# Optimization experiments

Measured on AMD Instinct MI355X. Metric: run time of the kernel, lower is better.

The kernel has to match this reference:

```python
import jax, jax.numpy as jnp
import numpy as np

# Longformer-base-like config, 4 layers, seq 2048, one-sided window 256 (attention_window=512)
B, S, DM, H, L, FF, V, WIN = 1, 2048, 768, 12, 4, 3072, 50265, 256


def _ln(x, s, b):
    m = x.mean(-1, keepdims=True)
    v = ((x - m) ** 2).mean(-1, keepdims=True)
    return (x - m) * jax.lax.rsqrt(v + 1e-5) * s + b


def setup_inputs() -> dict:
    key = jax.random.key(0)
    ks = iter(jax.random.split(key, 48))
    nrm = lambda shape: jax.random.normal(next(ks), shape, jnp.float32) * 0.02
    z = lambda shape: jnp.zeros(shape, jnp.float32)
    o = lambda shape: jnp.ones(shape, jnp.float32)
    return {
        'src': jax.random.randint(next(ks), (B, S), 0, V),
        'mask_src': jnp.ones((B, S), jnp.int32),
        'cluster_sizes': jax.random.randint(next(ks), (B,), 1, 10),
        'emb_word': nrm((V, DM)), 'emb_pos': nrm((S + 2, DM)),
        'ln_emb_s': o((DM,)), 'ln_emb_b': z((DM,)),
        'Wq': nrm((L, DM, DM)), 'bq': z((L, DM)),
        'Wk': nrm((L, DM, DM)), 'bk': z((L, DM)),
        'Wv': nrm((L, DM, DM)), 'bv': z((L, DM)),
        'Wo': nrm((L, DM, DM)), 'bo': z((L, DM)),
        'Wqg': nrm((L, DM, DM)), 'bqg': z((L, DM)),
        'Wkg': nrm((L, DM, DM)), 'bkg': z((L, DM)),
        'Wvg': nrm((L, DM, DM)), 'bvg': z((L, DM)),
        'ln1_s': o((L, DM)), 'ln1_b': z((L, DM)),
        'Wff1': nrm((L, DM, FF)), 'bff1': z((L, FF)),
        'Wff2': nrm((L, FF, DM)), 'bff2': z((L, DM)),
        'ln2_s': o((L, DM)), 'ln2_b': z((L, DM)),
        'Wcls': nrm((DM,)), 'bcls': z(()),
    }


def _encode(src, mask_src, emb_word, emb_pos, ln_emb_s, ln_emb_b,
            Wq, bq, Wk, bk, Wv, bv, Wo, bo, Wqg, bqg, Wkg, bkg, Wvg, bvg,
            ln1_s, ln1_b, Wff1, bff1, Wff2, bff2, ln2_s, ln2_b):
    Dh = DM // H
    NC = S // WIN  # number of query chunks
    NEG = jnp.float32(-1e9)
    scale = jnp.float32(1.0 / np.sqrt(Dh))
    mask_f = mask_src.astype(jnp.float32)

    # RoBERTa-style embeddings (positions offset by padding_idx+1 = 2)
    x = _ln(emb_word[src] + emb_pos[jnp.arange(S) + 2][None], ln_emb_s, ln_emb_b)

    # Banded gather indices: chunk c of W queries sees 3W keys [c*W - W, c*W + 2W)
    idx = jnp.arange(NC)[:, None] * WIN + jnp.arange(3 * WIN)[None, :]  # [NC,3W] into padded seq
    j_abs = idx - WIN                                                   # absolute key positions
    qi = jnp.arange(NC)[:, None] * WIN + jnp.arange(WIN)[None, :]       # [NC,W] absolute query pos
    rel = j_abs[:, None, :] - qi[:, :, None]                            # [NC,W,3W]
    in_band = (jnp.abs(rel) <= WIN) & (j_abs[:, None, :] >= 0) & (j_abs[:, None, :] < S)
    # keys removed from windowed attention: padding tokens and global tokens (position 0)
    key_ok = mask_f * (jnp.arange(S)[None, :] != 0)                     # [B,S]
    kmb = jnp.pad(key_ok, ((0, 0), (WIN, WIN)))[:, idx]                 # [B,NC,3W]
    band_ok = in_band[None, None] & (kmb[:, None, :, None, :] > 0)      # [B,1,NC,W,3W]

    for l in range(L):
        heads = lambda Wm, bm: (x @ Wm[l] + bm[l]).reshape(B, S, H, Dh).transpose(0, 2, 1, 3)
        q = heads(Wq, bq) * scale                                       # [B,H,S,Dh]
        k = heads(Wk, bk)
        v = heads(Wv, bv)
        kb = jnp.pad(k, ((0, 0), (0, 0), (WIN, WIN), (0, 0)))[:, :, idx]  # [B,H,NC,3W,Dh]
        vb = jnp.pad(v, ((0, 0), (0, 0), (WIN, WIN), (0, 0)))[:, :, idx]
        band = jnp.einsum('bhcqd,bhckd->bhcqk', q.reshape(B, H, NC, WIN, Dh), kb)
        band = jnp.where(band_ok, band, NEG)
        # every query also attends the global key (position 0) via the regular k/v
        sg = jnp.einsum('bhsd,bhd->bhs', q, k[:, :, 0])
        sg = jnp.where((mask_f[:, 0] > 0)[:, None, None], sg, NEG).reshape(B, H, NC, WIN, 1)
        probs = jax.nn.softmax(jnp.concatenate([sg, band], axis=-1), axis=-1)
        pg = probs[..., 0].reshape(B, H, S)
        out = jnp.einsum('bhcqk,bhckd->bhcqd', probs[..., 1:], vb).reshape(B, H, S, Dh)
        out = out + pg[..., None] * v[:, :, 0][:, :, None, :]
        # global query token (position 0): full attention using the *_global projections
        qg = ((x[:, 0] @ Wqg[l] + bqg[l]).reshape(B, H, Dh)) * scale
        kg = heads(Wkg, bkg)
        vg = heads(Wvg, bvg)
        sgl = jnp.where(mask_f[:, None, :] > 0, jnp.einsum('bhd,bhsd->bhs', qg, kg), NEG)
        og = jnp.einsum('bhs,bhsd->bhd', jax.nn.softmax(sgl, axis=-1), vg)
        out = out.at[:, :, 0].set(og)
        ctx = out.transpose(0, 2, 1, 3).reshape(B, S, DM)
        x = _ln(x + ctx @ Wo[l] + bo[l], ln1_s[l], ln1_b[l])
        ff = jax.nn.gelu(x @ Wff1[l] + bff1[l], approximate=False) @ Wff2[l] + bff2[l]
        x = _ln(x + ff, ln2_s[l], ln2_b[l])
    return x


def reference(src, mask_src, cluster_sizes, emb_word, emb_pos, ln_emb_s, ln_emb_b,
              Wq, bq, Wk, bk, Wv, bv, Wo, bo, Wqg, bqg, Wkg, bkg, Wvg, bvg,
              ln1_s, ln1_b, Wff1, bff1, Wff2, bff2, ln2_s, ln2_b, Wcls, bcls):
    x = _encode(src, mask_src, emb_word, emb_pos, ln_emb_s, ln_emb_b,
                Wq, bq, Wk, bk, Wv, bv, Wo, bo, Wqg, bqg, Wkg, bkg, Wvg, bvg,
                ln1_s, ln1_b, Wff1, bff1, Wff2, bff2, ln2_s, ln2_b)
    mask0 = mask_src[:, 0].astype(jnp.float32)
    scores = jax.nn.sigmoid(x[:, 0] @ Wcls + bcls) * mask0  # Classifier on CLS embedding
    return scores[:, None], mask_src[:, 0][:, None]
```

## Files before the change

### kernel.cpp

```cpp
#include <hip/hip_runtime.h>
#include <hip/hip_bf16.h>
#include <math.h>

#define S_LEN 2048
#define DMODEL 768
#define NHEAD 12
#define DHEAD 64
#define NLAYER 4
#define FFDIM 3072
#define WINSZ 256

typedef unsigned short u16;
typedef __attribute__((ext_vector_type(8))) short bfrag;
typedef __attribute__((ext_vector_type(4))) float ffrag;

static __device__ __forceinline__ int detect_bf16(const unsigned* flagp) {
    return flagp[0] != 0x3F800000u;
}

static __device__ __forceinline__ float ldin(const void* p, long i, int bf) {
    return bf ? __bfloat162float(((const __hip_bfloat16*)p)[i])
              : ((const float*)p)[i];
}

static __device__ __forceinline__ u16 f2bf(float v) {
    unsigned u = __float_as_uint(v);
    unsigned r = (u + 0x7FFFu + ((u >> 16) & 1u)) >> 16;
    return (u16)r;
}

static __device__ __forceinline__ float bf2f(u16 v) {
    return __uint_as_float((unsigned)v << 16);
}

static __device__ __forceinline__ void async16(const u16* g, u16* l) {
#if __has_builtin(__builtin_amdgcn_global_load_lds)
    __builtin_amdgcn_global_load_lds(
        (const __attribute__((address_space(1))) void*)g,
        (__attribute__((address_space(3))) void*)l, 16, 0, 0);
#else
    *(int4*)l = *(const int4*)g;
#endif
}

static __device__ __forceinline__ void blk_reduce_sum2(float& a, float& b) {
    __shared__ float sred[8];
    #pragma unroll
    for (int off = 32; off; off >>= 1) {
        a += __shfl_down(a, off);
        b += __shfl_down(b, off);
    }
    int lane = threadIdx.x & 63, w = threadIdx.x >> 6;
    if (lane == 0) { sred[w] = a; sred[w + 4] = b; }
    __syncthreads();
    a = sred[0] + sred[1] + sred[2] + sred[3];
    b = sred[4] + sred[5] + sred[6] + sred[7];
    __syncthreads();
}

struct T6Args { const void* w[6]; };

__global__ __launch_bounds__(256)
void transpose_w6_kernel(T6Args args, u16* __restrict__ Wt,
                         const unsigned* __restrict__ flagp) {
    int bf = detect_bf16(flagp);
    int z = blockIdx.z;
    const void* W = args.w[z >> 2];
    long so = (long)(z & 3) * DMODEL * DMODEL;
    long dofs = (long)z * DMODEL * DMODEL;
    int n0 = blockIdx.x * 64, k0 = blockIdx.y * 64;
    __shared__ float t[64][65];
    int tid = threadIdx.x;
    #pragma unroll
    for (int r = 0; r < 16; ++r) {
        int idx = r * 256 + tid;
        int k = idx >> 6, n = idx & 63;
        t[k][n] = ldin(W, so + (long)(k0 + k) * DMODEL + n0 + n, bf);
    }
    __syncthreads();
    #pragma unroll
    for (int r = 0; r < 16; ++r) {
        int idx = r * 256 + tid;
        int n = idx >> 6, k = idx & 63;
        Wt[dofs + (long)(n0 + n) * DMODEL + k0 + k] = f2bf(t[k][n]);
    }
}

__global__ __launch_bounds__(256)
void transpose_w_kernel(const void* __restrict__ W, u16* __restrict__ Wt,
                        int K, int N, const unsigned* __restrict__ flagp) {
    int bf = detect_bf16(flagp);
    long zo = (long)blockIdx.z * K * N;
    int n0 = blockIdx.x * 64, k0 = blockIdx.y * 64;
    __shared__ float t[64][65];
    int tid = threadIdx.x;
    #pragma unroll
    for (int r = 0; r < 16; ++r) {
        int idx = r * 256 + tid;
        int k = idx >> 6, n = idx & 63;
        t[k][n] = ldin(W, zo + (long)(k0 + k) * N + n0 + n, bf);
    }
    __syncthreads();
    #pragma unroll
    for (int r = 0; r < 16; ++r) {
        int idx = r * 256 + tid;
        int n = idx >> 6, k = idx & 63;
        Wt[zo + (long)(n0 + n) * K + k0 + k] = f2bf(t[k][n]);
    }
}

__global__ __launch_bounds__(256)
void embed_kernel(const int* __restrict__ src, const void* __restrict__ emb_word,
                  const void* __restrict__ emb_pos, const void* __restrict__ ln_s,
                  const void* __restrict__ ln_b, float* __restrict__ X,
                  u16* __restrict__ Xb, const unsigned* __restrict__ flagp) {
    int bf = detect_bf16(flagp);
    int s = blockIdx.x;
    int tid = threadIdx.x;
    int tok = src[s];
    float e[3];
    #pragma unroll
    for (int i = 0; i < 3; ++i) {
        int d = tid + i * 256;
        e[i] = ldin(emb_word, (long)tok * DMODEL + d, bf)
             + ldin(emb_pos, (long)(s + 2) * DMODEL + d, bf);
    }
    float sum = e[0] + e[1] + e[2];
    float sq  = e[0]*e[0] + e[1]*e[1] + e[2]*e[2];
    blk_reduce_sum2(sum, sq);
    float mean = sum * (1.0f / DMODEL);
    float var  = sq * (1.0f / DMODEL) - mean * mean;
    float inv  = rsqrtf(var + 1e-5f);
    #pragma unroll
    for (int i = 0; i < 3; ++i) {
        int d = tid + i * 256;
        float v = (e[i] - mean) * inv * ldin(ln_s, d, bf) + ldin(ln_b, d, bf);
        X[(long)s * DMODEL + d] = v;
        Xb[(long)s * DMODEL + d] = f2bf(v);
    }
}

__global__ __launch_bounds__(256)
void ln_res2_kernel(float* __restrict__ X, const float* __restrict__ T0,
                    const float* __restrict__ T1,
                    const void* __restrict__ ln_s, long soff,
                    const void* __restrict__ ln_b, long boff,
                    u16* __restrict__ Xb, const unsigned* __restrict__ flagp) {
    int bf = detect_bf16(flagp);
    int s = blockIdx.x;
    int tid = threadIdx.x;
    float e[3];
    #pragma unroll
    for (int i = 0; i < 3; ++i) {
        long d = (long)s * DMODEL + tid + i * 256;
        e[i] = X[d] + T0[d] + T1[d];
    }
    float sum = e[0] + e[1] + e[2];
    float sq  = e[0]*e[0] + e[1]*e[1] + e[2]*e[2];
    blk_reduce_sum2(sum, sq);
    float mean = sum * (1.0f / DMODEL);
    float var  = sq * (1.0f / DMODEL) - mean * mean;
    float inv  = rsqrtf(var + 1e-5f);
    #pragma unroll
    for (int i = 0; i < 3; ++i) {
        int d = tid + i * 256;
        float v = (e[i] - mean) * inv * ldin(ln_s, soff + d, bf) + ldin(ln_b, boff + d, bf);
        X[(long)s * DMODEL + d] = v;
        Xb[(long)s * DMODEL + d] = f2bf(v);
    }
}

static __device__ __forceinline__ void gemm_body(
    const u16* __restrict__ A, int lda, const u16* __restrict__ Wt, int ldb,
    const void* __restrict__ bias, long boff, int bf,
    float* __restrict__ outF, u16* __restrict__ outB, u16* __restrict__ outBT, int ldt,
    int N, int klen, float alpha, int gelu,
    u16 (*As)[32], u16 (*Bs)[32], int bm, int bn)
{
    int tid = threadIdx.x;
    int wave = tid >> 6, lane = tid & 63;
    int quad = lane >> 4, l15 = lane & 15;
    int wm = (wave >> 1) * 64, wn = (wave & 1) * 64;

    int srow = wave * 16 + (lane >> 2);
    int scol = (lane & 3) * 8;
    const u16* Ag0 = A  + (long)(bm + srow) * lda + scol;
    const u16* Ag1 = A  + (long)(bm + 64 + srow) * lda + scol;
    const u16* Bg0 = Wt + (long)(bn + srow) * ldb + scol;
    const u16* Bg1 = Wt + (long)(bn + 64 + srow) * ldb + scol;
    u16* Al0 = &As[srow][scol];
    u16* Al1 = &As[64 + srow][scol];
    u16* Bl0 = &Bs[srow][scol];
    u16* Bl1 = &Bs[64 + srow][scol];

    ffrag zero = {0.f, 0.f, 0.f, 0.f};
    ffrag acc[4][4];
    #pragma unroll
    for (int mi = 0; mi < 4; ++mi)
        #pragma unroll
        for (int ni = 0; ni < 4; ++ni) acc[mi][ni] = zero;

    for (int k0 = 0; k0 < klen; k0 += 32) {
        __syncthreads();
        async16(Ag0 + k0, Al0);
        async16(Ag1 + k0, Al1);
        async16(Bg0 + k0, Bl0);
        async16(Bg1 + k0, Bl1);
        __syncthreads();
        bfrag af[4], bfr[4];
        #pragma unroll
        for (int mi = 0; mi < 4; ++mi)
            af[mi] = *(const bfrag*)&As[wm + mi * 16 + l15][quad * 8];
        #pragma unroll
        for (int ni = 0; ni < 4; ++ni)
            bfr[ni] = *(const bfrag*)&Bs[wn + ni * 16 + l15][quad * 8];
        #pragma unroll
        for (int mi = 0; mi < 4; ++mi)
            #pragma unroll
            for (int ni = 0; ni < 4; ++ni)
                acc[mi][ni] = __builtin_amdgcn_mfma_f32_16x16x32_bf16(
                    af[mi], bfr[ni], acc[mi][ni], 0, 0, 0);
    }

    #pragma unroll
    for (int mi = 0; mi < 4; ++mi) {
        #pragma unroll
        for (int ni = 0; ni < 4; ++ni) {
            int row0 = bm + wm + mi * 16 + quad * 4;
            int col  = bn + wn + ni * 16 + l15;
            float bb = bias ? ldin(bias, boff + col, bf) : 0.0f;
            float v[4];
            #pragma unroll
            for (int i = 0; i < 4; ++i) {
                float x = (acc[mi][ni][i] + bb) * alpha;
                if (gelu) x = 0.5f * x * (1.0f + erff(x * 0.70710678118f));
                v[i] = x;
            }
            if (outF) {
                #pragma unroll
                for (int i = 0; i < 4; ++i) outF[(long)(row0 + i) * N + col] = v[i];
            }
            if (outB) {
                #pragma unroll
                for (int i = 0; i < 4; ++i) outB[(long)(row0 + i) * N + col] = f2bf(v[i]);
            }
            if (outBT) {
                ushort4 pk;
                pk.x = f2bf(v[0]); pk.y = f2bf(v[1]); pk.z = f2bf(v[2]); pk.w = f2bf(v[3]);
                *(ushort4*)&outBT[(long)col * ldt + row0] = pk;
            }
        }
    }
}

__global__ __launch_bounds__(256)
void gemm_one_kernel(const u16* __restrict__ A, int lda, const u16* __restrict__ Wt, int ldb,
                     const void* __restrict__ bias, long boff,
                     float* __restrict__ outF, long ofstride, u16* __restrict__ outB,
                     int N, int klen, float alpha, int gelu,
                     const unsigned* __restrict__ flagp) {
    __shared__ __align__(16) u16 As[128][32];
    __shared__ __align__(16) u16 Bs[128][32];
    long kbeg = (long)blockIdx.z * klen;
    gemm_body(A + kbeg, lda, Wt + kbeg, ldb,
              blockIdx.z == 0 ? bias : nullptr, boff, detect_bf16(flagp),
              outF ? outF + blockIdx.z * ofstride : nullptr, outB, nullptr, 0,
              N, klen, alpha, gelu, As, Bs, blockIdx.x * 128, blockIdx.y * 128);
}

struct Qkv5Args {
    const u16* wt[5];
    const void* bias[5];
    u16* outB[5];
    u16* outBT[5];
};

__global__ __launch_bounds__(256)
void gemm_qkv5_kernel(const u16* __restrict__ A, Qkv5Args args, long boff,
                      const unsigned* __restrict__ flagp) {
    __shared__ __align__(16) u16 As[128][32];
    __shared__ __align__(16) u16 Bs[128][32];
    int z = blockIdx.z;
    float alpha = (z == 0) ? 0.125f : 1.0f;
    gemm_body(A, DMODEL, args.wt[z], DMODEL, args.bias[z], boff, detect_bf16(flagp),
              nullptr, args.outB[z], args.outBT[z], S_LEN,
              DMODEL, DMODEL, alpha, 0,
              As, Bs, blockIdx.x * 128, blockIdx.y * 128);
}

__global__ __launch_bounds__(256)
void qg_kernel(const float* __restrict__ X, const void* __restrict__ W, long woff,
               float* __restrict__ QGp, const unsigned* __restrict__ flagp) {
    int bf = detect_bf16(flagp);
    int colb = blockIdx.x * 128, kb = blockIdx.y * 96;
    int cl = threadIdx.x & 127, kh = threadIdx.x >> 7;
    int col = colb + cl;
    __shared__ float xs[96];
    __shared__ float acc2[128];
    if (threadIdx.x < 96) xs[threadIdx.x] = X[kb + threadIdx.x];
    __syncthreads();
    float a = 0.0f;
    #pragma unroll 4
    for (int k = kh * 48; k < kh * 48 + 48; ++k)
        a = fmaf(xs[k], ldin(W, woff + (long)(kb + k) * DMODEL + col, bf), a);
    if (kh) acc2[cl] = a;
    __syncthreads();
    if (!kh) QGp[(long)blockIdx.y * DMODEL + col] = a + acc2[cl];
}

__global__ __launch_bounds__(256)
void band_mfma_kernel(const u16* __restrict__ Qb, const u16* __restrict__ Kb,
                      const u16* __restrict__ Vtg, u16* __restrict__ CTXb) {
    int qt = blockIdx.x, h = blockIdx.y;
    int q0 = qt * 64;
    int tid = threadIdx.x;
    int wave = tid >> 6, lane = tid & 63;
    int quad = lane >> 4, l15 = lane & 15;

    __shared__ __align__(16) u16 Qs[64][72];
    __shared__ __align__(16) u16 Ks[64][72];
    __shared__ __align__(16) u16 Vs[64][72];
    __shared__ __align__(16) float Pb[4][16][68];
    __shared__ __align__(16) u16 k0s[64];
    __shared__ __align__(16) u16 v0s[64];

    {
        int r = tid >> 2, seg = tid & 3;
        const u16* gq = Qb + (long)(q0 + r) * DMODEL + h * DHEAD + seg * 16;
        *(int4*)&Qs[r][seg * 16]     = *(const int4*)gq;
        *(int4*)&Qs[r][seg * 16 + 8] = *(const int4*)(gq + 8);
        if (tid < 8) *(int4*)&k0s[tid * 8] = *(const int4*)(Kb + h * DHEAD + tid * 8);
        if (tid >= 64 && tid < 128) {
            int d = tid - 64;
            v0s[d] = Vtg[(long)(h * DHEAD + d) * S_LEN];
        }
    }
    __syncthreads();

    float part = 0.0f;
    #pragma unroll
    for (int j = 0; j < 16; ++j)
        part = fmaf(bf2f(Qs[wave * 16 + l15][quad * 16 + j]), bf2f(k0s[quad * 16 + j]), part);
    part += __shfl_xor(part, 16);
    part += __shfl_xor(part, 32);
    float m = part, l = 1.0f;

    ffrag O4[4];
    #pragma unroll
    for (int dt = 0; dt < 4; ++dt) {
        float vv = bf2f(v0s[dt * 16 + l15]);
        ffrag t = {vv, vv, vv, vv};
        O4[dt] = t;
    }

    bfrag bq[2];
    bq[0] = *(const bfrag*)&Qs[wave * 16 + l15][quad * 8];
    bq[1] = *(const bfrag*)&Qs[wave * 16 + l15][32 + quad * 8];

    int q_abs = q0 + wave * 16 + l15;
    float (*Pw)[68] = Pb[wave];

    for (int t = 0; t < 9; ++t) {
        int jb = q0 - 256 + t * 64;
        if (jb < 0 || jb >= S_LEN) continue;

        __syncthreads();
        {
            int r = tid >> 2, seg = tid & 3;
            const u16* gk = Kb + (long)(jb + r) * DMODEL + h * DHEAD + seg * 16;
            *(int4*)&Ks[r][seg * 16]     = *(const int4*)gk;
            *(int4*)&Ks[r][seg * 16 + 8] = *(const int4*)(gk + 8);
            const u16* gv = Vtg + (long)(h * DHEAD + r) * S_LEN + jb + seg * 16;
            *(int4*)&Vs[r][seg * 16]     = *(const int4*)gv;
            *(int4*)&Vs[r][seg * 16 + 8] = *(const int4*)(gv + 8);
        }
        __syncthreads();

        ffrag sa[4];
        #pragma unroll
        for (int mt = 0; mt < 4; ++mt) {
            bfrag a0 = *(const bfrag*)&Ks[mt * 16 + l15][quad * 8];
            bfrag a1 = *(const bfrag*)&Ks[mt * 16 + l15][32 + quad * 8];
            ffrag z = {0.f, 0.f, 0.f, 0.f};
            z = __builtin_amdgcn_mfma_f32_16x16x32_bf16(a0, bq[0], z, 0, 0, 0);
            z = __builtin_amdgcn_mfma_f32_16x16x32_bf16(a1, bq[1], z, 0, 0, 0);
            sa[mt] = z;
        }

        float mx = -3e38f;
        #pragma unroll
        for (int mt = 0; mt < 4; ++mt) {
            #pragma unroll
            for (int reg = 0; reg < 4; ++reg) {
                int key = jb + mt * 16 + quad * 4 + reg;
                int rel = key - q_abs;
                bool ok = (key >= 1) && (rel >= -WINSZ) && (rel <= WINSZ);
                float s = ok ? sa[mt][reg] : -1e30f;
                sa[mt][reg] = s;
                mx = fmaxf(mx, s);
            }
        }
        mx = fmaxf(mx, __shfl_xor(mx, 16));
        mx = fmaxf(mx, __shfl_xor(mx, 32));
        float m_new = fmaxf(m, mx);
        float alpha = __expf(m - m_new);

        float rs = 0.0f;
        #pragma unroll
        for (int mt = 0; mt < 4; ++mt) {
            #pragma unroll
            for (int reg = 0; reg < 4; ++reg) {
                float p = __expf(sa[mt][reg] - m_new);
                sa[mt][reg] = p;
                rs += p;
            }
        }
        rs += __shfl_xor(rs, 16);
        rs += __shfl_xor(rs, 32);
        l = l * alpha + rs;
        m = m_new;

        #pragma unroll
        for (int mt = 0; mt < 4; ++mt)
            #pragma unroll
            for (int reg = 0; reg < 4; ++reg)
                Pw[l15][mt * 16 + quad * 4 + reg] = sa[mt][reg];

        float a4[4];
        #pragma unroll
        for (int reg = 0; reg < 4; ++reg)
            a4[reg] = __shfl(alpha, (lane & 48) + quad * 4 + reg);

        bfrag pa[2];
        #pragma unroll
        for (int ks = 0; ks < 2; ++ks) {
            float4 f0 = *(const float4*)&Pw[l15][ks * 32 + quad * 8];
            float4 f1 = *(const float4*)&Pw[l15][ks * 32 + quad * 8 + 4];
            union { bfrag v; short s[8]; } pu;
            pu.s[0] = (short)f2bf(f0.x); pu.s[1] = (short)f2bf(f0.y);
            pu.s[2] = (short)f2bf(f0.z); pu.s[3] = (short)f2bf(f0.w);
            pu.s[4] = (short)f2bf(f1.x); pu.s[5] = (short)f2bf(f1.y);
            pu.s[6] = (short)f2bf(f1.z); pu.s[7] = (short)f2bf(f1.w);
            pa[ks] = pu.v;
        }

        #pragma unroll
        for (int dt = 0; dt < 4; ++dt) {
            bfrag v0f = *(const bfrag*)&Vs[dt * 16 + l15][quad * 8];
            bfrag v1f = *(const bfrag*)&Vs[dt * 16 + l15][32 + quad * 8];
            ffrag o = O4[dt];
            #pragma unroll
            for (int reg = 0; reg < 4; ++reg) o[reg] *= a4[reg];
            o = __builtin_amdgcn_mfma_f32_16x16x32_bf16(pa[0], v0f, o, 0, 0, 0);
            o = __builtin_amdgcn_mfma_f32_16x16x32_bf16(pa[1], v1f, o, 0, 0, 0);
            O4[dt] = o;
        }
    }

    float l4[4];
    #pragma unroll
    for (int reg = 0; reg < 4; ++reg)
        l4[reg] = __shfl(l, (lane & 48) + quad * 4 + reg);

    #pragma unroll
    for (int dt = 0; dt < 4; ++dt) {
        #pragma unroll
        for (int reg = 0; reg < 4; ++reg) {
            int row = q0 + wave * 16 + quad * 4 + reg;
            CTXb[(long)row * DMODEL + h * DHEAD + dt * 16 + l15] = f2bf(O4[dt][reg] / l4[reg]);
        }
    }
}

__global__ __launch_bounds__(256)
void gattn_part_kernel(const float* __restrict__ QGp, const void* __restrict__ bqg, long boff,
                       const u16* __restrict__ KG, const u16* __restrict__ VG,
                       float* __restrict__ Gml, float* __restrict__ GO,
                       const unsigned* __restrict__ flagp) {
    int h = blockIdx.x, ck = blockIdx.y;
    int tid = threadIdx.x;
    int bf = detect_bf16(flagp);
    __shared__ float qs[DHEAD];
    __shared__ float sc[256];
    __shared__ float red[4];
    __shared__ float pt[4][DHEAD];

    if (tid < DHEAD) {
        float a = 0.0f;
        #pragma unroll
        for (int z = 0; z < 8; ++z) a += QGp[(long)z * DMODEL + h * DHEAD + tid];
        qs[tid] = (a + ldin(bqg, boff + h * DHEAD + tid, bf)) * 0.125f;
    }
    __syncthreads();

    int s = ck * 256 + tid;
    const int4* kp = (const int4*)(KG + (long)s * DMODEL + h * DHEAD);
    float dsum = 0.0f;
    #pragma unroll
    for (int i = 0; i < 8; ++i) {
        int4 raw = kp[i];
        const u16* pr = (const u16*)&raw;
        #pragma unroll
        for (int j = 0; j < 8; ++j) dsum = fmaf(qs[i * 8 + j], bf2f(pr[j]), dsum);
    }
    sc[tid] = dsum;
    float v = dsum;
    #pragma unroll
    for (int off = 32; off; off >>= 1) v = fmaxf(v, __shfl_down(v, off));
    if ((tid & 63) == 0) red[tid >> 6] = v;
    __syncthreads();
    float M = fmaxf(fmaxf(red[0], red[1]), fmaxf(red[2], red[3]));
    __syncthreads();
    float e = __expf(dsum - M);
    sc[tid] = e;
    float sum = e;
    #pragma unroll
    for (int off = 32; off; off >>= 1) sum += __shfl_down(sum, off);
    if ((tid & 63) == 0) red[tid >> 6] = sum;
    __syncthreads();
    float L = red[0] + red[1] + red[2] + red[3];

    int g = tid >> 6, dd = tid & 63;
    float acc = 0.0f;
    for (int j = g * 64; j < g * 64 + 64; ++j)
        acc = fmaf(sc[j], bf2f(VG[(long)(ck * 256 + j) * DMODEL + h * DHEAD + dd]), acc);
    pt[g][dd] = acc;
    __syncthreads();
    if (tid < DHEAD)
        GO[((long)h * 8 + ck) * DHEAD + tid] = pt[0][tid] + pt[1][tid] + pt[2][tid] + pt[3][tid];
    if (tid == 0) {
        Gml[((long)h * 8 + ck) * 2]     = M;
        Gml[((long)h * 8 + ck) * 2 + 1] = L;
    }
}

__global__ __launch_bounds__(64)
void gattn_combine_kernel(const float* __restrict__ Gml, const float* __restrict__ GO,
                          u16* __restrict__ CTXb) {
    int h = blockIdx.x, d = threadIdx.x;
    float M = -3e38f;
    #pragma unroll
    for (int z = 0; z < 8; ++z) M = fmaxf(M, Gml[((long)h * 8 + z) * 2]);
    float L = 0.0f, O = 0.0f;
    #pragma unroll
    for (int z = 0; z < 8; ++z) {
        float w = __expf(Gml[((long)h * 8 + z) * 2] - M);
        L += Gml[((long)h * 8 + z) * 2 + 1] * w;
        O = fmaf(GO[((long)h * 8 + z) * DHEAD + d], w, O);
    }
    CTXb[h * DHEAD + d] = f2bf(O / L);
}

__global__ __launch_bounds__(256)
void cls_kernel(const float* __restrict__ X, const void* __restrict__ Wcls,
                const void* __restrict__ bcls, const int* __restrict__ mask_src,
                void* __restrict__ out, const unsigned* __restrict__ flagp) {
    int bf = detect_bf16(flagp);
    int tid = threadIdx.x;
    float a = 0.0f, dummy = 0.0f;
    #pragma unroll
    for (int i = 0; i < 3; ++i) {
        int d = tid + i * 256;
        a = fmaf(X[d], ldin(Wcls, d, bf), a);
    }
    blk_reduce_sum2(a, dummy);
    if (tid == 0) {
        float z = a + ldin(bcls, 0, bf);
        float scr = 1.0f / (1.0f + __expf(-z));
        float mk = (float)mask_src[0];
        scr *= mk;
        if (bf) {
            __hip_bfloat16* o = (__hip_bfloat16*)out;
            o[0] = __float2bfloat16(scr);
            o[1] = __float2bfloat16(mk);
        } else {
            float* o = (float*)out;
            o[0] = scr;
            o[1] = mk;
        }
    }
}

extern "C" void kernel_launch(void* const* d_in, const int* in_sizes, int n_in,
                              void* d_out, int out_size, void* d_ws, size_t ws_size,
                              hipStream_t stream) {
    (void)in_sizes; (void)n_in; (void)out_size; (void)ws_size;
    const int* src       = (const int*)d_in[0];
    const int* mask_src  = (const int*)d_in[1];
    const void* emb_word = d_in[3];
    const void* emb_pos  = d_in[4];
    const unsigned* flagp = (const unsigned*)d_in[5];
    const void* ln_emb_s = d_in[5];
    const void* ln_emb_b = d_in[6];

    char* base = (char*)d_ws;
    size_t off = 0;
    auto carve = [&](size_t bytes) {
        void* p = base + off;
        off = (off + bytes + 255) & ~(size_t)255;
        return p;
    };
    const long DD = (long)DMODEL * DMODEL;
    const long DF = (long)DMODEL * FFDIM;
    const long SD = (long)S_LEN * DMODEL;
    const long SF = (long)S_LEN * FFDIM;

    u16* W6    = (u16*)carve(6 * NLAYER * DD * 2);
    u16* FF1T  = (u16*)carve(NLAYER * DF * 2);
    u16* FF2T  = (u16*)carve(NLAYER * DF * 2);
    float* X   = (float*)carve(SD * 4);
    float* TMP0 = (float*)carve(SD * 4);
    float* TMP1 = (float*)carve(SD * 4);
    u16* Xb    = (u16*)carve(SD * 2);
    u16* Qb16  = (u16*)carve(SD * 2);
    u16* Kb16  = (u16*)carve(SD * 2);
    u16* Vtg   = (u16*)carve(SD * 2);
    u16* KGb16 = (u16*)carve(SD * 2);
    u16* VGb16 = (u16*)carve(SD * 2);
    u16* CTXb  = (u16*)carve(SD * 2);
    u16* FF1b  = (u16*)carve(SF * 2);
    float* QGp = (float*)carve(8 * DMODEL * 4);
    float* Gml = (float*)carve(NHEAD * 8 * 2 * 4);
    float* GO  = (float*)carve(NHEAD * 8 * DHEAD * 4);

    T6Args t6;
    t6.w[0] = d_in[7];  t6.w[1] = d_in[9];  t6.w[2] = d_in[11];
    t6.w[3] = d_in[17]; t6.w[4] = d_in[19]; t6.w[5] = d_in[13];
    transpose_w6_kernel<<<dim3(12, 12, 24), 256, 0, stream>>>(t6, W6, flagp);
    transpose_w_kernel<<<dim3(48, 12, NLAYER), 256, 0, stream>>>(d_in[23], FF1T, DMODEL, FFDIM, flagp);
    transpose_w_kernel<<<dim3(12, 48, NLAYER), 256, 0, stream>>>(d_in[25], FF2T, FFDIM, DMODEL, flagp);

    embed_kernel<<<S_LEN, 256, 0, stream>>>(src, emb_word, emb_pos, ln_emb_s, ln_emb_b,
                                            X, Xb, flagp);

    for (int l = 0; l < NLAYER; ++l) {
        long wo  = (long)l * DD;
        long bo  = (long)l * DMODEL;
        long b1o = (long)l * FFDIM;

        Qkv5Args qa;
        qa.wt[0] = W6 + (0L * NLAYER + l) * DD; qa.bias[0] = d_in[8];  qa.outB[0] = Qb16;  qa.outBT[0] = nullptr;
        qa.wt[1] = W6 + (1L * NLAYER + l) * DD; qa.bias[1] = d_in[10]; qa.outB[1] = Kb16;  qa.outBT[1] = nullptr;
        qa.wt[2] = W6 + (2L * NLAYER + l) * DD; qa.bias[2] = d_in[12]; qa.outB[2] = nullptr; qa.outBT[2] = Vtg;
        qa.wt[3] = W6 + (3L * NLAYER + l) * DD; qa.bias[3] = d_in[18]; qa.outB[3] = KGb16; qa.outBT[3] = nullptr;
        qa.wt[4] = W6 + (4L * NLAYER + l) * DD; qa.bias[4] = d_in[20]; qa.outB[4] = VGb16; qa.outBT[4] = nullptr;
        gemm_qkv5_kernel<<<dim3(16, 6, 5), 256, 0, stream>>>(Xb, qa, bo, flagp);

        qg_kernel<<<dim3(6, 8), 256, 0, stream>>>(X, d_in[15], wo, QGp, flagp);

        band_mfma_kernel<<<dim3(32, NHEAD), 256, 0, stream>>>(Qb16, Kb16, Vtg, CTXb);
        gattn_part_kernel<<<dim3(NHEAD, 8), 256, 0, stream>>>(QGp, d_in[16], bo, KGb16, VGb16,
                                                              Gml, GO, flagp);
        gattn_combine_kernel<<<NHEAD, 64, 0, stream>>>(Gml, GO, CTXb);

        gemm_one_kernel<<<dim3(16, 6, 2), 256, 0, stream>>>(
            CTXb, DMODEL, W6 + (5L * NLAYER + l) * DD, DMODEL, d_in[14], bo,
            TMP0, SD, nullptr, DMODEL, 384, 1.0f, 0, flagp);
        ln_res2_kernel<<<S_LEN, 256, 0, stream>>>(X, TMP0, TMP1, d_in[21], bo, d_in[22], bo, Xb, flagp);

        gemm_one_kernel<<<dim3(16, 24, 1), 256, 0, stream>>>(
            Xb, DMODEL, FF1T + (long)l * DF, DMODEL, d_in[24], b1o,
            nullptr, 0, FF1b, FFDIM, DMODEL, 1.0f, 1, flagp);
        gemm_one_kernel<<<dim3(16, 6, 2), 256, 0, stream>>>(
            FF1b, FFDIM, FF2T + (long)l * DF, FFDIM, d_in[26], bo,
            TMP0, SD, nullptr, DMODEL, 1536, 1.0f, 0, flagp);
        ln_res2_kernel<<<S_LEN, 256, 0, stream>>>(X, TMP0, TMP1, d_in[27], bo, d_in[28], bo, Xb, flagp);
    }

    cls_kernel<<<1, 256, 0, stream>>>(X, d_in[29], d_in[30], mask_src, d_out, flagp);
}
```

Baseline: 1.087 ms.

## Fuse attention kernels, transposes, global-combine and classifier to cut launches

Merges the three weight-transpose launches into one flat-grid kernel. Merges the query-global projection, banded attention and global partial attention into a single kernel that uses a shared-memory union. The global-attention combine is folded into the Wo GEMM as a patch of row 0 of the A tile, and the classifier is folded into the final layernorm. This removes several small kernel launches and serial dependencies per layer, at the cost of extra branches and syncthreads inside the GEMM loop and a serial global-q projection inside each global block.

```diff
diff --git a/kernel.cpp b/kernel.cpp
--- a/kernel.cpp
+++ b/kernel.cpp
@@ -58,54 +58,45 @@
     __syncthreads();
 }
 
-struct T6Args { const void* w[6]; };
+struct TAllArgs { const void* w[8]; u16* d6; u16* d1; u16* d2; };
 
 __global__ __launch_bounds__(256)
-void transpose_w6_kernel(T6Args args, u16* __restrict__ Wt,
-                         const unsigned* __restrict__ flagp) {
+void transpose_all_kernel(TAllArgs args, const unsigned* __restrict__ flagp) {
     int bf = detect_bf16(flagp);
-    int z = blockIdx.z;
-    const void* W = args.w[z >> 2];
-    long so = (long)(z & 3) * DMODEL * DMODEL;
-    long dofs = (long)z * DMODEL * DMODEL;
-    int n0 = blockIdx.x * 64, k0 = blockIdx.y * 64;
+    const long DD = (long)DMODEL * DMODEL;
+    const long DF = (long)DMODEL * FFDIM;
+    int bid = blockIdx.x;
+    const void* srcp; u16* dst; int K, N, n0, k0; long so, dofs;
+    if (bid < 3456) {
+        int z = bid / 144, t = bid % 144;
+        srcp = args.w[z >> 2]; so = (long)(z & 3) * DD;
+        dst = args.d6; dofs = (long)z * DD;
+        K = DMODEL; N = DMODEL; n0 = (t % 12) * 64; k0 = (t / 12) * 64;
+    } else if (bid < 5760) {
+        int i = bid - 3456, layer = i / 576, t = i % 576;
+        srcp = args.w[6]; so = (long)layer * DF;
+        dst = args.d1; dofs = (long)layer * DF;
+        K = DMODEL; N = FFDIM; n0 = (t % 48) * 64; k0 = (t / 48) * 64;
+    } else {
+        int i = bid - 5760, layer = i / 576, t = i % 576;
+        srcp = args.w[7]; so = (long)layer * DF;
+        dst = args.d2; dofs = (long)layer * DF;
+        K = FFDIM; N = DMODEL; n0 = (t % 12) * 64; k0 = (t / 12) * 64;
+    }
     __shared__ float t[64][65];
     int tid = threadIdx.x;
     #pragma unroll
     for (int r = 0; r < 16; ++r) {
         int idx = r * 256 + tid;
         int k = idx >> 6, n = idx & 63;
-        t[k][n] = ldin(W, so + (long)(k0 + k) * DMODEL + n0 + n, bf);
+        t[k][n] = ldin(srcp, so + (long)(k0 + k) * N + n0 + n, bf);
     }
     __syncthreads();
     #pragma unroll
     for (int r = 0; r < 16; ++r) {
         int idx = r * 256 + tid;
         int n = idx >> 6, k = idx & 63;
-        Wt[dofs + (long)(n0 + n) * DMODEL + k0 + k] = f2bf(t[k][n]);
-    }
-}
-
-__global__ __launch_bounds__(256)
-void transpose_w_kernel(const void* __restrict__ W, u16* __restrict__ Wt,
-                        int K, int N, const unsigned* __restrict__ flagp) {
-    int bf = detect_bf16(flagp);
-    long zo = (long)blockIdx.z * K * N;
-    int n0 = blockIdx.x * 64, k0 = blockIdx.y * 64;
-    __shared__ float t[64][65];
-    int tid = threadIdx.x;
-    #pragma unroll
-    for (int r = 0; r < 16; ++r) {
-        int idx = r * 256 + tid;
-        int k = idx >> 6, n = idx & 63;
-        t[k][n] = ldin(W, zo + (long)(k0 + k) * N + n0 + n, bf);
-    }
-    __syncthreads();
-    #pragma unroll
-    for (int r = 0; r < 16; ++r) {
-        int idx = r * 256 + tid;
-        int n = idx >> 6, k = idx & 63;
-        Wt[zo + (long)(n0 + n) * K + k0 + k] = f2bf(t[k][n]);
+        dst[dofs + (long)(n0 + n) * K + k0 + k] = f2bf(t[k][n]);
     }
 }
 
@@ -145,7 +136,10 @@
                     const float* __restrict__ T1,
                     const void* __restrict__ ln_s, long soff,
                     const void* __restrict__ ln_b, long boff,
-                    u16* __restrict__ Xb, const unsigned* __restrict__ flagp) {
+                    u16* __restrict__ Xb, const unsigned* __restrict__ flagp,
+                    int do_cls, const void* __restrict__ Wcls,
+                    const void* __restrict__ bcls, const int* __restrict__ mask_src,
+                    void* __restrict__ out) {
     int bf = detect_bf16(flagp);
     int s = blockIdx.x;
     int tid = threadIdx.x;
@@ -161,12 +155,36 @@
     float mean = sum * (1.0f / DMODEL);
     float var  = sq * (1.0f / DMODEL) - mean * mean;
     float inv  = rsqrtf(var + 1e-5f);
+    float v3[3];
     #pragma unroll
     for (int i = 0; i < 3; ++i) {
         int d = tid + i * 256;
         float v = (e[i] - mean) * inv * ldin(ln_s, soff + d, bf) + ldin(ln_b, boff + d, bf);
+        v3[i] = v;
         X[(long)s * DMODEL + d] = v;
         Xb[(long)s * DMODEL + d] = f2bf(v);
+    }
+    if (do_cls && s == 0) {
+        float a = 0.0f, dummy = 0.0f;
+        #pragma unroll
+        for (int i = 0; i < 3; ++i)
+            a = fmaf(v3[i], ldin(Wcls, tid + i * 256, bf), a);
+        blk_reduce_sum2(a, dummy);
+        if (tid == 0) {
+            float z = a + ldin(bcls, 0, bf);
+            float scr = 1.0f / (1.0f + __expf(-z));
+            float mk = (float)mask_src[0];
+            scr *= mk;
+            if (bf) {
+                __hip_bfloat16* o = (__hip_bfloat16*)out;
+                o[0] = __float2bfloat16(scr);
+                o[1] = __float2bfloat16(mk);
+            } else {
+                float* o = (float*)out;
+                o[0] = scr;
+                o[1] = mk;
+            }
+        }
     }
 }
 
@@ -175,7 +193,8 @@
     const void* __restrict__ bias, long boff, int bf,
     float* __restrict__ outF, u16* __restrict__ outB, u16* __restrict__ outBT, int ldt,
     int N, int klen, float alpha, int gelu,
-    u16 (*As)[32], u16 (*Bs)[32], int bm, int bn)
+    u16 (*As)[32], u16 (*Bs)[32], int bm, int bn,
+    int patch_mode, const u16* __restrict__ ctx0s, long kbeg)
 {
     int tid = threadIdx.x;
     int wave = tid >> 6, lane = tid & 63;
@@ -207,6 +226,14 @@
         async16(Bg0 + k0, Bl0);
         async16(Bg1 + k0, Bl1);
         __syncthreads();
+        if (patch_mode) {
+            if (bm == 0 && tid < 4) {
+                #pragma unroll
+                for (int j = 0; j < 8; ++j)
+                    As[0][tid * 8 + j] = ctx0s[kbeg + k0 + tid * 8 + j];
+            }
+            __syncthreads();
+        }
         bfrag af[4], bfr[4];
         #pragma unroll
         for (int mi = 0; mi < 4; ++mi)
@@ -258,14 +285,35 @@
                      const void* __restrict__ bias, long boff,
                      float* __restrict__ outF, long ofstride, u16* __restrict__ outB,
                      int N, int klen, float alpha, int gelu,
+                     const float* __restrict__ Gml, const float* __restrict__ GO,
                      const unsigned* __restrict__ flagp) {
     __shared__ __align__(16) u16 As[128][32];
     __shared__ __align__(16) u16 Bs[128][32];
+    __shared__ __align__(16) u16 ctx0s[DMODEL];
+    int patch = (Gml != nullptr);
+    int bm = blockIdx.x * 128;
+    if (patch && bm == 0) {
+        for (int i = threadIdx.x; i < DMODEL; i += 256) {
+            int h = i >> 6, d = i & 63;
+            float M = -3e38f;
+            #pragma unroll
+            for (int z = 0; z < 8; ++z) M = fmaxf(M, Gml[((long)h * 8 + z) * 2]);
+            float L = 0.f, O = 0.f;
+            #pragma unroll
+            for (int z = 0; z < 8; ++z) {
+                float w = __expf(Gml[((long)h * 8 + z) * 2] - M);
+                L += Gml[((long)h * 8 + z) * 2 + 1] * w;
+                O = fmaf(GO[((long)h * 8 + z) * DHEAD + d], w, O);
+            }
+            ctx0s[i] = f2bf(O / L);
+        }
+    }
     long kbeg = (long)blockIdx.z * klen;
     gemm_body(A + kbeg, lda, Wt + kbeg, ldb,
               blockIdx.z == 0 ? bias : nullptr, boff, detect_bf16(flagp),
               outF ? outF + blockIdx.z * ofstride : nullptr, outB, nullptr, 0,
-              N, klen, alpha, gelu, As, Bs, blockIdx.x * 128, blockIdx.y * 128);
+              N, klen, alpha, gelu, As, Bs, bm, blockIdx.y * 128,
+              patch, ctx0s, kbeg);
 }
 
 struct Qkv5Args {
@@ -285,298 +333,250 @@
     gemm_body(A, DMODEL, args.wt[z], DMODEL, args.bias[z], boff, detect_bf16(flagp),
               nullptr, args.outB[z], args.outBT[z], S_LEN,
               DMODEL, DMODEL, alpha, 0,
-              As, Bs, blockIdx.x * 128, blockIdx.y * 128);
-}
+              As, Bs, blockIdx.x * 128, blockIdx.y * 128, 0, nullptr, 0);
+}
+
+struct BandShared {
+    u16 Qs[64][72];
+    u16 Ks[64][72];
+    u16 Vs[64][72];
+    float Pb[4][16][68];
+    u16 k0s[64];
+    u16 v0s[64];
+};
+struct GattnShared {
+    float xs[DMODEL];
+    float qs[DHEAD];
+    float sc[256];
+    float red[4];
+    float pt[4][DHEAD];
+};
+union AttnShared { BandShared b; GattnShared g; };
 
 __global__ __launch_bounds__(256)
-void qg_kernel(const float* __restrict__ X, const void* __restrict__ W, long woff,
-               float* __restrict__ QGp, const unsigned* __restrict__ flagp) {
-    int bf = detect_bf16(flagp);
-    int colb = blockIdx.x * 128, kb = blockIdx.y * 96;
-    int cl = threadIdx.x & 127, kh = threadIdx.x >> 7;
-    int col = colb + cl;
-    __shared__ float xs[96];
-    __shared__ float acc2[128];
-    if (threadIdx.x < 96) xs[threadIdx.x] = X[kb + threadIdx.x];
-    __syncthreads();
-    float a = 0.0f;
-    #pragma unroll 4
-    for (int k = kh * 48; k < kh * 48 + 48; ++k)
-        a = fmaf(xs[k], ldin(W, woff + (long)(kb + k) * DMODEL + col, bf), a);
-    if (kh) acc2[cl] = a;
-    __syncthreads();
-    if (!kh) QGp[(long)blockIdx.y * DMODEL + col] = a + acc2[cl];
-}
-
-__global__ __launch_bounds__(256)
-void band_mfma_kernel(const u16* __restrict__ Qb, const u16* __restrict__ Kb,
-                      const u16* __restrict__ Vtg, u16* __restrict__ CTXb) {
-    int qt = blockIdx.x, h = blockIdx.y;
-    int q0 = qt * 64;
-    int tid = threadIdx.x;
-    int wave = tid >> 6, lane = tid & 63;
-    int quad = lane >> 4, l15 = lane & 15;
-
-    __shared__ __align__(16) u16 Qs[64][72];
-    __shared__ __align__(16) u16 Ks[64][72];
-    __shared__ __align__(16) u16 Vs[64][72];
-    __shared__ __align__(16) float Pb[4][16][68];
-    __shared__ __align__(16) u16 k0s[64];
-    __shared__ __align__(16) u16 v0s[64];
-
-    {
-        int r = tid >> 2, seg = tid & 3;
-        const u16* gq = Qb + (long)(q0 + r) * DMODEL + h * DHEAD + seg * 16;
-        *(int4*)&Qs[r][seg * 16]     = *(const int4*)gq;
-        *(int4*)&Qs[r][seg * 16 + 8] = *(const int4*)(gq + 8);
-        if (tid < 8) *(int4*)&k0s[tid * 8] = *(const int4*)(Kb + h * DHEAD + tid * 8);
-        if (tid >= 64 && tid < 128) {
-            int d = tid - 64;
-            v0s[d] = Vtg[(long)(h * DHEAD + d) * S_LEN];
-        }
-    }
-    __syncthreads();
-
-    float part = 0.0f;
-    #pragma unroll
-    for (int j = 0; j < 16; ++j)
-        part = fmaf(bf2f(Qs[wave * 16 + l15][quad * 16 + j]), bf2f(k0s[quad * 16 + j]), part);
-    part += __shfl_xor(part, 16);
-    part += __shfl_xor(part, 32);
-    float m = part, l = 1.0f;
-
-    ffrag O4[4];
-    #pragma unroll
-    for (int dt = 0; dt < 4; ++dt) {
-        float vv = bf2f(v0s[dt * 16 + l15]);
-        ffrag t = {vv, vv, vv, vv};
-        O4[dt] = t;
-    }
-
-    bfrag bq[2];
-    bq[0] = *(const bfrag*)&Qs[wave * 16 + l15][quad * 8];
-    bq[1] = *(const bfrag*)&Qs[wave * 16 + l15][32 + quad * 8];
-
-    int q_abs = q0 + wave * 16 + l15;
-    float (*Pw)[68] = Pb[wave];
-
-    for (int t = 0; t < 9; ++t) {
-        int jb = q0 - 256 + t * 64;
-        if (jb < 0 || jb >= S_LEN) continue;
-
-        __syncthreads();
-        {
-            int r = tid >> 2, seg = tid & 3;
-            const u16* gk = Kb + (long)(jb + r) * DMODEL + h * DHEAD + seg * 16;
-            *(int4*)&Ks[r][seg * 16]     = *(const int4*)gk;
-            *(int4*)&Ks[r][seg * 16 + 8] = *(const int4*)(gk + 8);
-            const u16* gv = Vtg + (long)(h * DHEAD + r) * S_LEN + jb + seg * 16;
-            *(int4*)&Vs[r][seg * 16]     = *(const int4*)gv;
-            *(int4*)&Vs[r][seg * 16 + 8] = *(const int4*)(gv + 8);
-        }
-        __syncthreads();
-
-        ffrag sa[4];
-        #pragma unroll
-        for (int mt = 0; mt < 4; ++mt) {
-            bfrag a0 = *(const bfrag*)&Ks[mt * 16 + l15][quad * 8];
-            bfrag a1 = *(const bfrag*)&Ks[mt * 16 + l15][32 + quad * 8];
-            ffrag z = {0.f, 0.f, 0.f, 0.f};
-            z = __builtin_amdgcn_mfma_f32_16x16x32_bf16(a0, bq[0], z, 0, 0, 0);
-            z = __builtin_amdgcn_mfma_f32_16x16x32_bf16(a1, bq[1], z, 0, 0, 0);
-            sa[mt] = z;
-        }
-
-        float mx = -3e38f;
-        #pragma unroll
-        for (int mt = 0; mt < 4; ++mt) {
-            #pragma unroll
-            for (int reg = 0; reg < 4; ++reg) {
-                int key = jb + mt * 16 + quad * 4 + reg;
-                int rel = key - q_abs;
-                bool ok = (key >= 1) && (rel >= -WINSZ) && (rel <= WINSZ);
-                float s = ok ? sa[mt][reg] : -1e30f;
-                sa[mt][reg] = s;
-                mx = fmaxf(mx, s);
-            }
-        }
-        mx = fmaxf(mx, __shfl_xor(mx, 16));
-        mx = fmaxf(mx, __shfl_xor(mx, 32));
-        float m_new = fmaxf(m, mx);
-        float alpha = __expf(m - m_new);
-
-        float rs = 0.0f;
-        #pragma unroll
-        for (int mt = 0; mt < 4; ++mt) {
-            #pragma unroll
-            for (int reg = 0; reg < 4; ++reg) {
-                float p = __expf(sa[mt][reg] - m_new);
-                sa[mt][reg] = p;
-                rs += p;
-            }
-        }
-        rs += __shfl_xor(rs, 16);
-        rs += __shfl_xor(rs, 32);
-        l = l * alpha + rs;
-        m = m_new;
-
-        #pragma unroll
-        for (int mt = 0; mt < 4; ++mt)
-            #pragma unroll
-            for (int reg = 0; reg < 4; ++reg)
-                Pw[l15][mt * 16 + quad * 4 + reg] = sa[mt][reg];
-
-        float a4[4];
-        #pragma unroll
-        for (int reg = 0; reg < 4; ++reg)
-            a4[reg] = __shfl(alpha, (lane & 48) + quad * 4 + reg);
-
-        bfrag pa[2];
-        #pragma unroll
-        for (int ks = 0; ks < 2; ++ks) {
-            float4 f0 = *(const float4*)&Pw[l15][ks * 32 + quad * 8];
-            float4 f1 = *(const float4*)&Pw[l15][ks * 32 + quad * 8 + 4];
-            union { bfrag v; short s[8]; } pu;
-            pu.s[0] = (short)f2bf(f0.x); pu.s[1] = (short)f2bf(f0.y);
-            pu.s[2] = (short)f2bf(f0.z); pu.s[3] = (short)f2bf(f0.w);
-            pu.s[4] = (short)f2bf(f1.x); pu.s[5] = (short)f2bf(f1.y);
-            pu.s[6] = (short)f2bf(f1.z); pu.s[7] = (short)f2bf(f1.w);
-            pa[ks] = pu.v;
-        }
-
-        #pragma unroll
-        for (int dt = 0; dt < 4; ++dt) {
-            bfrag v0f = *(const bfrag*)&Vs[dt * 16 + l15][quad * 8];
-            bfrag v1f = *(const bfrag*)&Vs[dt * 16 + l15][32 + quad * 8];
-            ffrag o = O4[dt];
-            #pragma unroll
-            for (int reg = 0; reg < 4; ++reg) o[reg] *= a4[reg];
-            o = __builtin_amdgcn_mfma_f32_16x16x32_bf16(pa[0], v0f, o, 0, 0, 0);
-            o = __builtin_amdgcn_mfma_f32_16x16x32_bf16(pa[1], v1f, o, 0, 0, 0);
-            O4[dt] = o;
-        }
-    }
-
-    float l4[4];
-    #pragma unroll
-    for (int reg = 0; reg < 4; ++reg)
-        l4[reg] = __shfl(l, (lane & 48) + quad * 4 + reg);
-
-    #pragma unroll
-    for (int dt = 0; dt < 4; ++dt) {
-        #pragma unroll
-        for (int reg = 0; reg < 4; ++reg) {
-            int row = q0 + wave * 16 + quad * 4 + reg;
-            CTXb[(long)row * DMODEL + h * DHEAD + dt * 16 + l15] = f2bf(O4[dt][reg] / l4[reg]);
-        }
-    }
-}
-
-__global__ __launch_bounds__(256)
-void gattn_part_kernel(const float* __restrict__ QGp, const void* __restrict__ bqg, long boff,
+void attn_fused_kernel(const u16* __restrict__ Qb, const u16* __restrict__ Kb,
+                       const u16* __restrict__ Vtg, u16* __restrict__ CTXb,
+                       const float* __restrict__ X, const void* __restrict__ Wqg, long wo,
+                       const void* __restrict__ bqg, long bo,
                        const u16* __restrict__ KG, const u16* __restrict__ VG,
                        float* __restrict__ Gml, float* __restrict__ GO,
                        const unsigned* __restrict__ flagp) {
-    int h = blockIdx.x, ck = blockIdx.y;
+    __shared__ __align__(16) AttnShared sm;
+    int bid = blockIdx.x;
     int tid = threadIdx.x;
-    int bf = detect_bf16(flagp);
-    __shared__ float qs[DHEAD];
-    __shared__ float sc[256];
-    __shared__ float red[4];
-    __shared__ float pt[4][DHEAD];
-
-    if (tid < DHEAD) {
-        float a = 0.0f;
-        #pragma unroll
-        for (int z = 0; z < 8; ++z) a += QGp[(long)z * DMODEL + h * DHEAD + tid];
-        qs[tid] = (a + ldin(bqg, boff + h * DHEAD + tid, bf)) * 0.125f;
-    }
-    __syncthreads();
-
-    int s = ck * 256 + tid;
-    const int4* kp = (const int4*)(KG + (long)s * DMODEL + h * DHEAD);
-    float dsum = 0.0f;
-    #pragma unroll
-    for (int i = 0; i < 8; ++i) {
-        int4 raw = kp[i];
-        const u16* pr = (const u16*)&raw;
-        #pragma unroll
-        for (int j = 0; j < 8; ++j) dsum = fmaf(qs[i * 8 + j], bf2f(pr[j]), dsum);
-    }
-    sc[tid] = dsum;
-    float v = dsum;
-    #pragma unroll
-    for (int off = 32; off; off >>= 1) v = fmaxf(v, __shfl_down(v, off));
-    if ((tid & 63) == 0) red[tid >> 6] = v;
-    __syncthreads();
-    float M = fmaxf(fmaxf(red[0], red[1]), fmaxf(red[2], red[3]));
-    __syncthreads();
-    float e = __expf(dsum - M);
-    sc[tid] = e;
-    float sum = e;
-    #pragma unroll
-    for (int off = 32; off; off >>= 1) sum += __shfl_down(sum, off);
-    if ((tid & 63) == 0) red[tid >> 6] = sum;
-    __syncthreads();
-    float L = red[0] + red[1] + red[2] + red[3];
-
-    int g = tid >> 6, dd = tid & 63;
-    float acc = 0.0f;
-    for (int j = g * 64; j < g * 64 + 64; ++j)
-        acc = fmaf(sc[j], bf2f(VG[(long)(ck * 256 + j) * DMODEL + h * DHEAD + dd]), acc);
-    pt[g][dd] = acc;
-    __syncthreads();
-    if (tid < DHEAD)
-        GO[((long)h * 8 + ck) * DHEAD + tid] = pt[0][tid] + pt[1][tid] + pt[2][tid] + pt[3][tid];
-    if (tid == 0) {
-        Gml[((long)h * 8 + ck) * 2]     = M;
-        Gml[((long)h * 8 + ck) * 2 + 1] = L;
-    }
-}
-
-__global__ __launch_bounds__(64)
-void gattn_combine_kernel(const float* __restrict__ Gml, const float* __restrict__ GO,
-                          u16* __restrict__ CTXb) {
-    int h = blockIdx.x, d = threadIdx.x;
-    float M = -3e38f;
-    #pragma unroll
-    for (int z = 0; z < 8; ++z) M = fmaxf(M, Gml[((long)h * 8 + z) * 2]);
-    float L = 0.0f, O = 0.0f;
-    #pragma unroll
-    for (int z = 0; z < 8; ++z) {
-        float w = __expf(Gml[((long)h * 8 + z) * 2] - M);
-        L += Gml[((long)h * 8 + z) * 2 + 1] * w;
-        O = fmaf(GO[((long)h * 8 + z) * DHEAD + d], w, O);
-    }
-    CTXb[h * DHEAD + d] = f2bf(O / L);
-}
-
-__global__ __launch_bounds__(256)
-void cls_kernel(const float* __restrict__ X, const void* __restrict__ Wcls,
-                const void* __restrict__ bcls, const int* __restrict__ mask_src,
-                void* __restrict__ out, const unsigned* __restrict__ flagp) {
-    int bf = detect_bf16(flagp);
-    int tid = threadIdx.x;
-    float a = 0.0f, dummy = 0.0f;
-    #pragma unroll
-    for (int i = 0; i < 3; ++i) {
-        int d = tid + i * 256;
-        a = fmaf(X[d], ldin(Wcls, d, bf), a);
-    }
-    blk_reduce_sum2(a, dummy);
-    if (tid == 0) {
-        float z = a + ldin(bcls, 0, bf);
-        float scr = 1.0f / (1.0f + __expf(-z));
-        float mk = (float)mask_src[0];
-        scr *= mk;
-        if (bf) {
-            __hip_bfloat16* o = (__hip_bfloat16*)out;
-            o[0] = __float2bfloat16(scr);
-            o[1] = __float2bfloat16(mk);
-        } else {
-            float* o = (float*)out;
-            o[0] = scr;
-            o[1] = mk;
+
+    if (bid < 384) {
+        int qt = bid & 31, h = bid >> 5;
+        int q0 = qt * 64;
+        int wave = tid >> 6, lane = tid & 63;
+        int quad = lane >> 4, l15 = lane & 15;
+
+        {
+            int r = tid >> 2, seg = tid & 3;
+            const u16* gq = Qb + (long)(q0 + r) * DMODEL + h * DHEAD + seg * 16;
+            *(int4*)&sm.b.Qs[r][seg * 16]     = *(const int4*)gq;
+            *(int4*)&sm.b.Qs[r][seg * 16 + 8] = *(const int4*)(gq + 8);
+            if (tid < 8) *(int4*)&sm.b.k0s[tid * 8] = *(const int4*)(Kb + h * DHEAD + tid * 8);
+            if (tid >= 64 && tid < 128) {
+                int d = tid - 64;
+                sm.b.v0s[d] = Vtg[(long)(h * DHEAD + d) * S_LEN];
+            }
+        }
+        __syncthreads();
+
+        float part = 0.0f;
+        #pragma unroll
+        for (int j = 0; j < 16; ++j)
+            part = fmaf(bf2f(sm.b.Qs[wave * 16 + l15][quad * 16 + j]),
+                        bf2f(sm.b.k0s[quad * 16 + j]), part);
+        part += __shfl_xor(part, 16);
+        part += __shfl_xor(part, 32);
+        float m = part, l = 1.0f;
+
+        ffrag O4[4];
+        #pragma unroll
+        for (int dt = 0; dt < 4; ++dt) {
+            float vv = bf2f(sm.b.v0s[dt * 16 + l15]);
+            ffrag t = {vv, vv, vv, vv};
+            O4[dt] = t;
+        }
+
+        bfrag bq[2];
+        bq[0] = *(const bfrag*)&sm.b.Qs[wave * 16 + l15][quad * 8];
+        bq[1] = *(const bfrag*)&sm.b.Qs[wave * 16 + l15][32 + quad * 8];
+
+        int q_abs = q0 + wave * 16 + l15;
+        float (*Pw)[68] = sm.b.Pb[wave];
+
+        for (int t = 0; t < 9; ++t) {
+            int jb = q0 - 256 + t * 64;
+            if (jb < 0 || jb >= S_LEN) continue;
+
+            __syncthreads();
+            {
+                int r = tid >> 2, seg = tid & 3;
+                const u16* gk = Kb + (long)(jb + r) * DMODEL + h * DHEAD + seg * 16;
+                *(int4*)&sm.b.Ks[r][seg * 16]     = *(const int4*)gk;
+                *(int4*)&sm.b.Ks[r][seg * 16 + 8] = *(const int4*)(gk + 8);
+                const u16* gv = Vtg + (long)(h * DHEAD + r) * S_LEN + jb + seg * 16;
+                *(int4*)&sm.b.Vs[r][seg * 16]     = *(const int4*)gv;
+                *(int4*)&sm.b.Vs[r][seg * 16 + 8] = *(const int4*)(gv + 8);
+            }
+            __syncthreads();
+
+            ffrag sa[4];
+            #pragma unroll
+            for (int mt = 0; mt < 4; ++mt) {
+                bfrag a0 = *(const bfrag*)&sm.b.Ks[mt * 16 + l15][quad * 8];
+                bfrag a1 = *(const bfrag*)&sm.b.Ks[mt * 16 + l15][32 + quad * 8];
+                ffrag z = {0.f, 0.f, 0.f, 0.f};
+                z = __builtin_amdgcn_mfma_f32_16x16x32_bf16(a0, bq[0], z, 0, 0, 0);
+                z = __builtin_amdgcn_mfma_f32_16x16x32_bf16(a1, bq[1], z, 0, 0, 0);
+                sa[mt] = z;
+            }
+
+            float mx = -3e38f;
+            #pragma unroll
+            for (int mt = 0; mt < 4; ++mt) {
+                #pragma unroll
+                for (int reg = 0; reg < 4; ++reg) {
+                    int key = jb + mt * 16 + quad * 4 + reg;
+                    int rel = key - q_abs;
+                    bool ok = (key >= 1) && (rel >= -WINSZ) && (rel <= WINSZ);
+                    float s = ok ? sa[mt][reg] : -1e30f;
+                    sa[mt][reg] = s;
+                    mx = fmaxf(mx, s);
+                }
+            }
+            mx = fmaxf(mx, __shfl_xor(mx, 16));
+            mx = fmaxf(mx, __shfl_xor(mx, 32));
+            float m_new = fmaxf(m, mx);
+            float alpha = __expf(m - m_new);
+
+            float rs = 0.0f;
+            #pragma unroll
+            for (int mt = 0; mt < 4; ++mt) {
+                #pragma unroll
+                for (int reg = 0; reg < 4; ++reg) {
+                    float p = __expf(sa[mt][reg] - m_new);
+                    sa[mt][reg] = p;
+                    rs += p;
+                }
+            }
+            rs += __shfl_xor(rs, 16);
+            rs += __shfl_xor(rs, 32);
+            l = l * alpha + rs;
+            m = m_new;
+
+            #pragma unroll
+            for (int mt = 0; mt < 4; ++mt)
+                #pragma unroll
+                for (int reg = 0; reg < 4; ++reg)
+                    Pw[l15][mt * 16 + quad * 4 + reg] = sa[mt][reg];
+
+            float a4[4];
+            #pragma unroll
+            for (int reg = 0; reg < 4; ++reg)
+                a4[reg] = __shfl(alpha, (lane & 48) + quad * 4 + reg);
+
+            bfrag pa[2];
+            #pragma unroll
+            for (int ks = 0; ks < 2; ++ks) {
+                float4 f0 = *(const float4*)&Pw[l15][ks * 32 + quad * 8];
+                float4 f1 = *(const float4*)&Pw[l15][ks * 32 + quad * 8 + 4];
+                union { bfrag v; short s[8]; } pu;
+                pu.s[0] = (short)f2bf(f0.x); pu.s[1] = (short)f2bf(f0.y);
+                pu.s[2] = (short)f2bf(f0.z); pu.s[3] = (short)f2bf(f0.w);
+                pu.s[4] = (short)f2bf(f1.x); pu.s[5] = (short)f2bf(f1.y);
+                pu.s[6] = (short)f2bf(f1.z); pu.s[7] = (short)f2bf(f1.w);
+                pa[ks] = pu.v;
+            }
+
+            #pragma unroll
+            for (int dt = 0; dt < 4; ++dt) {
+                bfrag v0f = *(const bfrag*)&sm.b.Vs[dt * 16 + l15][quad * 8];
+                bfrag v1f = *(const bfrag*)&sm.b.Vs[dt * 16 + l15][32 + quad * 8];
+                ffrag o = O4[dt];
+                #pragma unroll
+                for (int reg = 0; reg < 4; ++reg) o[reg] *= a4[reg];
+                o = __builtin_amdgcn_mfma_f32_16x16x32_bf16(pa[0], v0f, o, 0, 0, 0);
+                o = __builtin_amdgcn_mfma_f32_16x16x32_bf16(pa[1], v1f, o, 0, 0, 0);
+                O4[dt] = o;
+            }
+        }
+
+        float l4[4];
+        #pragma unroll
+        for (int reg = 0; reg < 4; ++reg)
+            l4[reg] = __shfl(l, (lane & 48) + quad * 4 + reg);
+
+        #pragma unroll
+        for (int dt = 0; dt < 4; ++dt) {
+            #pragma unroll
+            for (int reg = 0; reg < 4; ++reg) {
+                int row = q0 + wave * 16 + quad * 4 + reg;
+                CTXb[(long)row * DMODEL + h * DHEAD + dt * 16 + l15] = f2bf(O4[dt][reg] / l4[reg]);
+            }
+        }
+    } else {
+        int bf = detect_bf16(flagp);
+        int idx = bid - 384;
+        int h = idx >> 3, ck = idx & 7;
+
+        for (int i = tid; i < DMODEL; i += 256) sm.g.xs[i] = X[i];
+        __syncthreads();
+        {
+            int d = tid & 63, part = tid >> 6;
+            float a = 0.0f;
+            for (int k = part * 192; k < part * 192 + 192; ++k)
+                a = fmaf(sm.g.xs[k], ldin(Wqg, wo + (long)k * DMODEL + h * DHEAD + d, bf), a);
+            sm.g.pt[part][d] = a;
+        }
+        __syncthreads();
+        if (tid < DHEAD)
+            sm.g.qs[tid] = ((sm.g.pt[0][tid] + sm.g.pt[1][tid] + sm.g.pt[2][tid] + sm.g.pt[3][tid])
+                            + ldin(bqg, bo + h * DHEAD + tid, bf)) * 0.125f;
+        __syncthreads();
+
+        int s = ck * 256 + tid;
+        const int4* kp = (const int4*)(KG + (long)s * DMODEL + h * DHEAD);
+        float dsum = 0.0f;
+        #pragma unroll
+        for (int i = 0; i < 8; ++i) {
+            int4 raw = kp[i];
+            const u16* pr = (const u16*)&raw;
+            #pragma unroll
+            for (int j = 0; j < 8; ++j) dsum = fmaf(sm.g.qs[i * 8 + j], bf2f(pr[j]), dsum);
+        }
+        sm.g.sc[tid] = dsum;
+        float v = dsum;
+        #pragma unroll
+        for (int off = 32; off; off >>= 1) v = fmaxf(v, __shfl_down(v, off));
+        if ((tid & 63) == 0) sm.g.red[tid >> 6] = v;
+        __syncthreads();
+        float M = fmaxf(fmaxf(sm.g.red[0], sm.g.red[1]), fmaxf(sm.g.red[2], sm.g.red[3]));
+        __syncthreads();
+        float e = __expf(dsum - M);
+        sm.g.sc[tid] = e;
+        float sum = e;
+        #pragma unroll
+        for (int off = 32; off; off >>= 1) sum += __shfl_down(sum, off);
+        if ((tid & 63) == 0) sm.g.red[tid >> 6] = sum;
+        __syncthreads();
+        float L = sm.g.red[0] + sm.g.red[1] + sm.g.red[2] + sm.g.red[3];
+
+        int g = tid >> 6, dd = tid & 63;
+        float acc = 0.0f;
+        for (int j = g * 64; j < g * 64 + 64; ++j)
+            acc = fmaf(sm.g.sc[j], bf2f(VG[(long)(ck * 256 + j) * DMODEL + h * DHEAD + dd]), acc);
+        sm.g.pt[g][dd] = acc;
+        __syncthreads();
+        if (tid < DHEAD)
+            GO[((long)h * 8 + ck) * DHEAD + tid] =
+                sm.g.pt[0][tid] + sm.g.pt[1][tid] + sm.g.pt[2][tid] + sm.g.pt[3][tid];
+        if (tid == 0) {
+            Gml[((long)h * 8 + ck) * 2]     = M;
+            Gml[((long)h * 8 + ck) * 2 + 1] = L;
         }
     }
 }
@@ -619,16 +619,15 @@
     u16* VGb16 = (u16*)carve(SD * 2);
     u16* CTXb  = (u16*)carve(SD * 2);
     u16* FF1b  = (u16*)carve(SF * 2);
-    float* QGp = (float*)carve(8 * DMODEL * 4);
     float* Gml = (float*)carve(NHEAD * 8 * 2 * 4);
     float* GO  = (float*)carve(NHEAD * 8 * DHEAD * 4);
 
-    T6Args t6;
-    t6.w[0] = d_in[7];  t6.w[1] = d_in[9];  t6.w[2] = d_in[11];
-    t6.w[3] = d_in[17]; t6.w[4] = d_in[19]; t6.w[5] = d_in[13];
-    transpose_w6_kernel<<<dim3(12, 12, 24), 256, 0, stream>>>(t6, W6, flagp);
-    transpose_w_kernel<<<dim3(48, 12, NLAYER), 256, 0, stream>>>(d_in[23], FF1T, DMODEL, FFDIM, flagp);
-    transpose_w_kernel<<<dim3(12, 48, NLAYER), 256, 0, stream>>>(d_in[25], FF2T, FFDIM, DMODEL, flagp);
+    TAllArgs ta;
+    ta.w[0] = d_in[7];  ta.w[1] = d_in[9];  ta.w[2] = d_in[11];
+    ta.w[3] = d_in[17]; ta.w[4] = d_in[19]; ta.w[5] = d_in[13];
+    ta.w[6] = d_in[23]; ta.w[7] = d_in[25];
+    ta.d6 = W6; ta.d1 = FF1T; ta.d2 = FF2T;
+    transpose_all_kernel<<<8064, 256, 0, stream>>>(ta, flagp);
 
     embed_kernel<<<S_LEN, 256, 0, stream>>>(src, emb_word, emb_pos, ln_emb_s, ln_emb_b,
                                             X, Xb, flagp);
@@ -646,26 +645,24 @@
         qa.wt[4] = W6 + (4L * NLAYER + l) * DD; qa.bias[4] = d_in[20]; qa.outB[4] = VGb16; qa.outBT[4] = nullptr;
         gemm_qkv5_kernel<<<dim3(16, 6, 5), 256, 0, stream>>>(Xb, qa, bo, flagp);
 
-        qg_kernel<<<dim3(6, 8), 256, 0, stream>>>(X, d_in[15], wo, QGp, flagp);
-
-        band_mfma_kernel<<<dim3(32, NHEAD), 256, 0, stream>>>(Qb16, Kb16, Vtg, CTXb);
-        gattn_part_kernel<<<dim3(NHEAD, 8), 256, 0, stream>>>(QGp, d_in[16], bo, KGb16, VGb16,
-                                                              Gml, GO, flagp);
-        gattn_combine_kernel<<<NHEAD, 64, 0, stream>>>(Gml, GO, CTXb);
+        attn_fused_kernel<<<480, 256, 0, stream>>>(Qb16, Kb16, Vtg, CTXb,
+                                                   X, d_in[15], wo, d_in[16], bo,
+                                                   KGb16, VGb16, Gml, GO, flagp);
 
         gemm_one_kernel<<<dim3(16, 6, 2), 256, 0, stream>>>(
             CTXb, DMODEL, W6 + (5L * NLAYER + l) * DD, DMODEL, d_in[14], bo,
-            TMP0, SD, nullptr, DMODEL, 384, 1.0f, 0, flagp);
-        ln_res2_kernel<<<S_LEN, 256, 0, stream>>>(X, TMP0, TMP1, d_in[21], bo, d_in[22], bo, Xb, flagp);
+            TMP0, SD, nullptr, DMODEL, 384, 1.0f, 0, Gml, GO, flagp);
+        ln_res2_kernel<<<S_LEN, 256, 0, stream>>>(X, TMP0, TMP1, d_in[21], bo, d_in[22], bo,
+                                                  Xb, flagp, 0, nullptr, nullptr, nullptr, nullptr);
 
         gemm_one_kernel<<<dim3(16, 24, 1), 256, 0, stream>>>(
             Xb, DMODEL, FF1T + (long)l * DF, DMODEL, d_in[24], b1o,
-            nullptr, 0, FF1b, FFDIM, DMODEL, 1.0f, 1, flagp);
+            nullptr, 0, FF1b, FFDIM, DMODEL, 1.0f, 1, nullptr, nullptr, flagp);
         gemm_one_kernel<<<dim3(16, 6, 2), 256, 0, stream>>>(
             FF1b, FFDIM, FF2T + (long)l * DF, FFDIM, d_in[26], bo,
-            TMP0, SD, nullptr, DMODEL, 1536, 1.0f, 0, flagp);
-        ln_res2_kernel<<<S_LEN, 256, 0, stream>>>(X, TMP0, TMP1, d_in[27], bo, d_in[28], bo, Xb, flagp);
-    }
-
-    cls_kernel<<<1, 256, 0, stream>>>(X, d_in[29], d_in[30], mask_src, d_out, flagp);
-}
+            TMP0, SD, nullptr, DMODEL, 1536, 1.0f, 0, nullptr, nullptr, flagp);
+        ln_res2_kernel<<<S_LEN, 256, 0, stream>>>(X, TMP0, TMP1, d_in[27], bo, d_in[28], bo,
+                                                  Xb, flagp, (l == NLAYER - 1) ? 1 : 0,
+                                                  d_in[29], d_in[30], mask_src, d_out);
+    }
+}
```

New measurement: 1.028 ms. 1.06x faster.
